# Kernel tuning notes

Measured on AMD Instinct MI355X. Metric: run time of the kernel, lower is better.

Reference implementation:

```python
import jax, jax.numpy as jnp
import numpy as np

K = 7        # upsample_kernel_size
S = 2        # upscale_factor
EK = K - 2   # encoder kernel size (5)


def conv2d(x, w, b, padding):
    out = jax.lax.conv_general_dilated(
        x, w, window_strides=(1, 1), padding=[(padding, padding), (padding, padding)],
        dimension_numbers=('NCHW', 'OIHW', 'NCHW'))
    return out + b[None, :, None, None]


def pixel_shuffle(x, s):
    B, C, H, W = x.shape
    oc = C // (s * s)
    x = x.reshape(B, oc, s, s, H, W)
    x = x.transpose(0, 1, 4, 2, 5, 3)
    return x.reshape(B, oc, H * s, W * s)


def carafe(x, kmap, k, s):
    # x: [B,C,H,W], kmap: [B,k*k,H*s,W*s] softmax-normalized
    B, C, H, W = x.shape
    pad = k // 2
    xp = jnp.pad(x, ((0, 0), (0, 0), (pad, pad), (pad, pad)))
    # k^2 shifted views -> [B,C,k2,H,W]
    patches = jnp.stack([xp[:, :, dy:dy + H, dx:dx + W]
                         for dy in range(k) for dx in range(k)], axis=2)
    # output pixel (i,j) reads source (i//s, j//s): factor kmap spatial dims
    km = kmap.reshape(B, k * k, H, s, W, s)
    out = jnp.einsum('bcnhw,bnhpwq->bchpwq', patches, km)
    return out.reshape(B, C, H * s, W * s)


def setup_inputs() -> dict:
    key = jax.random.key(0)
    k1, k2, k3 = jax.random.split(key, 3)
    B, C, H, W = 4, 256, 64, 64
    comp_c = 64
    enc_out = (S * K) ** 2  # 196
    x = jax.random.normal(k1, (B, C, H, W), dtype=jnp.float32)
    w_comp = jax.random.normal(k2, (comp_c, C, 1, 1), dtype=jnp.float32) * (1.0 / np.sqrt(C))
    b_comp = jnp.zeros((comp_c,), dtype=jnp.float32)
    w_enc = jax.random.normal(k3, (enc_out, comp_c, EK, EK), dtype=jnp.float32) * (1.0 / np.sqrt(comp_c * EK * EK))
    b_enc = jnp.zeros((enc_out,), dtype=jnp.float32)
    return {'x': x, 'w_comp': w_comp, 'b_comp': b_comp, 'w_enc': w_enc, 'b_enc': b_enc}


def reference(x, w_comp, b_comp, w_enc, b_enc):
    compressed = conv2d(x, w_comp, b_comp, padding=0)
    content = conv2d(compressed, w_enc, b_enc, padding=EK // 2)
    upsampled = pixel_shuffle(content, S)            # [B, k^2, H*s, W*s]
    kernel_map = jax.nn.softmax(upsampled, axis=1)
    return carafe(x, kernel_map, K, S)
```

## Files before the change

kernel.cpp:

```cpp
#include <hip/hip_runtime.h>
#include <math.h>
#include <stdint.h>

#define B_   4
#define C_   256
#define H_   64
#define W_   64
#define CC_  64
#define OE_  196
#define OH_  128
#define OW_  128
#define XH_  72
#define NWB_ 10

typedef uint32_t u32;
typedef unsigned short u16;
typedef __attribute__((ext_vector_type(8))) short bf16x8;
typedef __attribute__((ext_vector_type(4))) float f32x4;
typedef __attribute__((ext_vector_type(4))) u32 u32x4;
typedef __attribute__((ext_vector_type(2))) u32 u32x2;

__device__ __forceinline__ u16 f2bf(float f) {
  u32 u = __builtin_bit_cast(u32, f);
  u32 r = (u + 0x7FFFu + ((u >> 16) & 1u)) >> 16;
  return (u16)r;
}

__global__ __launch_bounds__(256) void prep_weights(
    const float* __restrict__ w_comp, const float* __restrict__ w_enc,
    u16* __restrict__ wfrag, u16* __restrict__ wcf,
    u16* __restrict__ xw8) {
  int idx = blockIdx.x * 256 + threadIdx.x;
  if (idx < 50 * 14 * 64) {
    int lane = idx & 63;
    int mt   = (idx >> 6) % 14;
    int ks   = idx / (14 * 64);
    int o    = mt * 16 + (lane & 15);
    int tap  = ks >> 1, s = ks & 1;
    int ky   = tap / 5, kx = tap % 5;
    int cb   = s * 32 + (lane >> 4) * 8;
    u32 pk[4];
    #pragma unroll
    for (int p = 0; p < 4; ++p) {
      u16 lo = 0, hi = 0;
      if (o < OE_) {
        lo = f2bf(w_enc[((o * CC_ + cb + 2 * p) * 5 + ky) * 5 + kx]);
        hi = f2bf(w_enc[((o * CC_ + cb + 2 * p + 1) * 5 + ky) * 5 + kx]);
      }
      pk[p] = (u32)lo | ((u32)hi << 16);
    }
    *reinterpret_cast<u32x4*>(wfrag + (size_t)idx * 8) =
        *reinterpret_cast<u32x4*>(pk);
  }
  if (idx < 8 * 4 * 64) {
    int lane = idx & 63;
    int mt   = (idx >> 6) & 3;
    int ks   = idx >> 8;
    int o    = mt * 16 + (lane & 15);
    int cb   = ks * 32 + (lane >> 4) * 8;
    u32 pk[4];
    #pragma unroll
    for (int p = 0; p < 4; ++p) {
      u16 lo = f2bf(w_comp[o * C_ + cb + 2 * p]);
      u16 hi = f2bf(w_comp[o * C_ + cb + 2 * p + 1]);
      pk[p] = (u32)lo | ((u32)hi << 16);
    }
    *reinterpret_cast<u32x4*>(wcf + (size_t)idx * 8) =
        *reinterpret_cast<u32x4*>(pk);
  }
  {
    u32x4 z = {0, 0, 0, 0};
    for (int i = idx; i < 1088 * 256; i += 65536) {
      int zi = i >> 8, ck = i & 255;
      int b = zi / 272, r = zi % 272;
      int hp, wb;
      if (r < 30)      { hp = r / 10;             wb = r % 10; }
      else if (r < 80) { hp = 67 + (r - 30) / 10; wb = (r - 30) % 10; }
      else {
        int rr = r - 80;
        hp = 3 + rr / 3;
        int m = rr % 3;
        wb = (m == 0) ? 0 : (m == 1) ? 8 : 9;
      }
      *reinterpret_cast<u32x4*>(
          xw8 + (((size_t)(b * XH_ + hp)) * NWB_ + wb) * (C_ * 8) + ck * 8) = z;
    }
  }
}

__global__ __launch_bounds__(256) void compress_k(
    const float* __restrict__ x, const u16* __restrict__ wcf,
    const float* __restrict__ b_comp, u16* __restrict__ comp,
    u16* __restrict__ xw8) {
  __shared__ float xs[C_ * 20];
  int t   = threadIdx.x;
  int gid = blockIdx.x;
  int wq  = gid & 3;
  int bh  = gid >> 2;
  int b = bh >> 6, h = bh & 63;
  int w0 = wq * 16;

  const float* xrow = x + (size_t)b * C_ * H_ * W_ + (size_t)h * W_ + w0;
  for (int i = t; i < 1024; i += 256) {
    int c = i >> 2, q = i & 3;
    f32x4 v = *reinterpret_cast<const f32x4*>(xrow + (size_t)c * H_ * W_ + q * 4);
    *reinterpret_cast<f32x4*>(xs + c * 20 + q * 4) = v;
  }
  __syncthreads();

  int wv   = __builtin_amdgcn_readfirstlane(t >> 6);
  int lane = t & 63;
  int w    = lane & 15;
  int lg   = lane >> 4;

  bf16x8 af[8];
  #pragma unroll
  for (int ks = 0; ks < 8; ++ks)
    af[ks] = *reinterpret_cast<const bf16x8*>(
        wcf + (((size_t)ks * 4 + wv) * 64 + lane) * 8);

  f32x4 acc = {0.f, 0.f, 0.f, 0.f};
  #pragma unroll
  for (int ks = 0; ks < 8; ++ks) {
    short vv[8];
    #pragma unroll
    for (int j = 0; j < 8; ++j)
      vv[j] = (short)f2bf(xs[(ks * 32 + lg * 8 + j) * 20 + w]);
    bf16x8 bf = (bf16x8){vv[0], vv[1], vv[2], vv[3], vv[4], vv[5], vv[6], vv[7]};
    acc = __builtin_amdgcn_mfma_f32_16x16x32_bf16(af[ks], bf, acc, 0, 0, 0);
  }

  {
    int cc0 = wv * 16 + lg * 4;
    f32x4 bias = *reinterpret_cast<const f32x4*>(b_comp + cc0);
    u32 p0 = (u32)f2bf(acc[0] + bias[0]) | ((u32)f2bf(acc[1] + bias[1]) << 16);
    u32 p1 = (u32)f2bf(acc[2] + bias[2]) | ((u32)f2bf(acc[3] + bias[3]) << 16);
    u32x2 pk = {p0, p1};
    *reinterpret_cast<u32x2*>(comp + ((size_t)bh * 64 + w0 + w) * CC_ + cc0) = pk;
  }

  {
    int ww = t & 15, cq = t >> 4;
    int wp = w0 + ww + 3;
    size_t base = (((size_t)(b * XH_ + h + 3)) * NWB_ + (wp >> 3)) * (C_ * 8) + (wp & 7);
    #pragma unroll
    for (int i = 0; i < 16; ++i) {
      int c = cq * 16 + i;
      xw8[base + c * 8] = f2bf(xs[c * 20 + ww]);
    }
  }
}

#define ELG_ 32256

__device__ __forceinline__ void enc_lda(
    bf16x8 (&a)[2], const u16* __restrict__ wfrag,
    int ks, int mtbase, int lane) {
  #pragma unroll
  for (int mm = 0; mm < 2; ++mm)
    a[mm] = *reinterpret_cast<const bf16x8*>(
        wfrag + (((size_t)ks * 14 + mtbase + mm) * 64 + lane) * 8);
}

__device__ __forceinline__ void enc_step(
    int ks, const char* lds, const bf16x8 (&a)[2], f32x4 (&acc)[2][2],
    int nlane, int kq) {
  int tap = ks >> 1, s = ks & 1;
  int ky = tap / 5, kx = tap % 5;
  bf16x8 bf[2];
  #pragma unroll
  for (int nt = 0; nt < 2; ++nt) {
    int col = nt * 16 + nlane + kx;
    int byte = (((ky * 36 + col) * 64 + s * 32 + kq * 8) * 2) ^ ((col & 7) << 4);
    bf[nt] = *reinterpret_cast<const bf16x8*>(lds + byte);
  }
  #pragma unroll
  for (int mm = 0; mm < 2; ++mm)
    #pragma unroll
    for (int nt = 0; nt < 2; ++nt)
      acc[mm][nt] = __builtin_amdgcn_mfma_f32_16x16x32_bf16(
          a[mm], bf[nt], acc[mm][nt], 0, 0, 0);
}

__global__ __launch_bounds__(512) void enc_mfma_k(
    const u16* __restrict__ comp, const u16* __restrict__ wfrag,
    const float* __restrict__ b_enc, u16* __restrict__ smax) {
  __shared__ __align__(16) char lds[ELG_];

  int t   = threadIdx.x;
  int bid = blockIdx.x;
  int swz = (bid & 7) * 64 + (bid >> 3);
  int wh  = swz & 1;
  int bh  = swz >> 1;
  int b = bh >> 6, h = bh & 63;
  int w0 = wh * 32;

  {
    const u16* cbse = comp + (size_t)b * H_ * W_ * CC_;
    for (int i = t; i < 1440; i += 512) {
      int q = i & 7, colr = i >> 3;
      int col = colr % 36, r = colr / 36;
      int hh = h - 2 + r, gw = w0 - 2 + col;
      u32x4 v = {0, 0, 0, 0};
      if ((unsigned)hh < H_ && (unsigned)gw < W_)
        v = *reinterpret_cast<const u32x4*>(cbse + ((size_t)hh * W_ + gw) * CC_ + q * 8);
      int byte = ((r * 36 + col) * 128 + q * 16) ^ ((col & 7) << 4);
      *reinterpret_cast<u32x4*>(lds + byte) = v;
    }
  }
  __syncthreads();

  int wv    = __builtin_amdgcn_readfirstlane(t >> 6);
  int lane  = t & 63;
  int nlane = lane & 15, kq = lane >> 4;
  int mtbase = wv * 2;

  f32x4 acc[2][2];
  #pragma unroll
  for (int mm = 0; mm < 2; ++mm)
    #pragma unroll
    for (int nt = 0; nt < 2; ++nt) acc[mm][nt] = (f32x4){0.f, 0.f, 0.f, 0.f};

  if (wv < 7) {
    bf16x8 abuf[4][2];
    #pragma unroll
    for (int p = 0; p < 4; ++p) enc_lda(abuf[p], wfrag, p, mtbase, lane);
    #pragma unroll
    for (int ks = 0; ks < 50; ++ks) {
      enc_step(ks, lds, abuf[ks & 3], acc, nlane, kq);
      if (ks < 46) enc_lda(abuf[ks & 3], wfrag, ks + 4, mtbase, lane);
    }
  }

  __syncthreads();
  float* lg = (float*)lds;
  if (wv < 7) {
    #pragma unroll
    for (int mm = 0; mm < 2; ++mm) {
      #pragma unroll
      for (int nt = 0; nt < 2; ++nt) {
        #pragma unroll
        for (int r = 0; r < 4; ++r) {
          int m  = (mtbase + mm) * 16 + kq * 4 + r;
          int px = nt * 16 + nlane;
          lg[m * 36 + px] = acc[mm][nt][r] + (m < OE_ ? b_enc[m] : 0.f);
        }
      }
    }
  }
  __syncthreads();

  if (t < 128) {
    int px = t & 31, rr = t >> 5;
    float v[49];
    float mx = -1e30f;
    #pragma unroll
    for (int n = 0; n < 49; ++n) {
      v[n] = lg[(4 * n + rr) * 36 + px];
      mx = fmaxf(mx, v[n]);
    }
    float sum = 0.f;
    #pragma unroll
    for (int n = 0; n < 49; ++n) { v[n] = __expf(v[n] - mx); sum += v[n]; }
    float inv = 1.f / sum;
    u16* so = smax + ((size_t)bh * 64 + w0 + px) * OE_;
    #pragma unroll
    for (int n = 0; n < 49; ++n) so[n * 4 + rr] = f2bf(v[n] * inv);
  }
}

__device__ __forceinline__ void carafe_lda(
    bf16x8 (&buf)[4], const u16* __restrict__ xb,
    int c, int h, int wb0, int lg) {
  #pragma unroll
  for (int ks = 0; ks < 4; ++ks) {
    int dy = ks * 2 + (lg >> 1);
    buf[ks] = *reinterpret_cast<const bf16x8*>(
        xb + (((size_t)(h + dy)) * NWB_ + wb0 + (lg & 1)) * (C_ * 8) + c * 8);
  }
}

__global__ __launch_bounds__(256) void carafe_k(
    const u16* __restrict__ xw8, const u16* __restrict__ smax,
    float* __restrict__ out) {
  __shared__ __align__(8) u16 svl[16 * 200];
  int t   = threadIdx.x;
  int bid = blockIdx.x;
  int swz = (bid & 7) * 256 + (bid >> 3);
  int mh  = swz & 1;
  int ws2 = (swz >> 1) & 3;
  int h   = (swz >> 3) & 63;
  int b   = swz >> 9;
  int w00 = ws2 * 16;

  for (int idx = t; idx < 784; idx += 256) {
    int pix = idx / 49, n = idx - pix * 49;
    const u16* sp = smax +
        ((size_t)((b * 64 + h) * 64) + w00 + pix) * OE_ + n * 4;
    *reinterpret_cast<u32x2*>(svl + pix * 200 + n * 4) =
        *reinterpret_cast<const u32x2*>(sp);
  }
  __syncthreads();

  int wv   = t >> 6;
  int lane = t & 63;
  int ws   = wv & 1;
  int mq   = wv >> 1;
  int w0   = w00 + ws * 8;
  int wb0  = w0 >> 3;
  const u16* svb = svl + ws * 8 * 200;

  int col = lane & 15;
  int wi  = col >> 1, q = col & 1;
  int lg  = lane >> 4;
  int mrow = lane & 15;

  bf16x8 bfr[2][4];
  #pragma unroll
  for (int p = 0; p < 2; ++p) {
    #pragma unroll
    for (int ks = 0; ks < 4; ++ks) {
      short v[8];
      #pragma unroll
      for (int j = 0; j < 8; ++j) {
        int k   = ks * 32 + lg * 8 + j;
        int dy  = k >> 4, dxp = k & 15;
        int dx  = dxp - wi;
        u16 s = 0;
        if (dy < 7 && dx >= 0 && dx < 7)
          s = svb[wi * 200 + (dy * 7 + dx) * 4 + 2 * p + q];
        v[j] = (short)s;
      }
      bfr[p][ks] = (bf16x8){v[0], v[1], v[2], v[3], v[4], v[5], v[6], v[7]};
    }
  }

  const u16* xb = xw8 + (size_t)b * XH_ * NWB_ * (C_ * 8);
  int mt0 = mh * 8 + mq * 4;
  bf16x8 buf[4][4];
  #pragma unroll
  for (int i = 0; i < 4; ++i)
    carafe_lda(buf[i], xb, (mt0 + i) * 16 + mrow, h, wb0, lg);

  #pragma unroll
  for (int i = 0; i < 4; ++i) {
    int mt = mt0 + i;
    f32x4 acc0 = {0.f, 0.f, 0.f, 0.f};
    f32x4 acc1 = {0.f, 0.f, 0.f, 0.f};
    #pragma unroll
    for (int ks = 0; ks < 4; ++ks) {
      acc0 = __builtin_amdgcn_mfma_f32_16x16x32_bf16(buf[i][ks], bfr[0][ks], acc0, 0, 0, 0);
      acc1 = __builtin_amdgcn_mfma_f32_16x16x32_bf16(buf[i][ks], bfr[1][ks], acc1, 0, 0, 0);
    }
    float* o0 = out +
        ((size_t)(b * C_ + mt * 16 + lg * 4) * OH_ + 2 * h) * OW_ + 2 * w0 + col;
    o0[0]                     = acc0[0];
    o0[(size_t)OH_ * OW_]     = acc0[1];
    o0[2 * (size_t)OH_ * OW_] = acc0[2];
    o0[3 * (size_t)OH_ * OW_] = acc0[3];
    float* o1 = o0 + OW_;
    o1[0]                     = acc1[0];
    o1[(size_t)OH_ * OW_]     = acc1[1];
    o1[2 * (size_t)OH_ * OW_] = acc1[2];
    o1[3 * (size_t)OH_ * OW_] = acc1[3];
  }
}

extern "C" void kernel_launch(void* const* d_in, const int* in_sizes, int n_in,
                              void* d_out, int out_size, void* d_ws, size_t ws_size,
                              hipStream_t stream) {
  const float* x      = (const float*)d_in[0];
  const float* w_comp = (const float*)d_in[1];
  const float* b_comp = (const float*)d_in[2];
  const float* w_enc  = (const float*)d_in[3];
  const float* b_enc  = (const float*)d_in[4];
  float* out = (float*)d_out;

  u16* smax  = (u16*)d_ws;
  u16* wfrag = smax + 3211264;
  u16* wcf   = wfrag + 358400;
  u16* comp  = wcf + 16384;
  u16* xw8   = comp + 1048576;

  prep_weights<<<256, 256, 0, stream>>>(w_comp, w_enc, wfrag, wcf, xw8);
  compress_k<<<B_ * H_ * 4, 256, 0, stream>>>(x, wcf, b_comp, comp, xw8);
  enc_mfma_k<<<512, 512, 0, stream>>>(comp, wfrag, b_enc, smax);
  carafe_k<<<2048, 256, 0, stream>>>(xw8, smax, out);
}
```

Before: 68.65 us.

## Emit MFMA-ready B fragments from encoder softmax and double-buffer carafe A loads

The encoder kernel now writes softmax weights directly in the per-lane bf16x8 fragment layout that carafe's MFMA B operand needs, expanding the 7x7 window into a zero-padded 16-wide band. This removes carafe's LDS staging, its barrier and the per-element gather logic. The cost is a larger workspace write (about 2.6x more data than the compact softmax) and an extra barrier in the encoder. Carafe also switches from preloading all four A tiles to a two-buffer prefetch, which lowers register pressure.

Result: faster. 65.68 us (-4.3%).

```diff
diff --git a/kernel.cpp b/kernel.cpp
--- a/kernel.cpp
+++ b/kernel.cpp
@@ -184,7 +184,7 @@
 
 __global__ __launch_bounds__(512) void enc_mfma_k(
     const u16* __restrict__ comp, const u16* __restrict__ wfrag,
-    const float* __restrict__ b_enc, u16* __restrict__ smax) {
+    const float* __restrict__ b_enc, u16* __restrict__ bfrB) {
   __shared__ __align__(16) char lds[ELG_];
 
   int t   = threadIdx.x;
@@ -250,9 +250,10 @@
   }
   __syncthreads();
 
+  float v[49];
+  float inv = 0.f;
   if (t < 128) {
     int px = t & 31, rr = t >> 5;
-    float v[49];
     float mx = -1e30f;
     #pragma unroll
     for (int n = 0; n < 49; ++n) {
@@ -262,95 +263,108 @@
     float sum = 0.f;
     #pragma unroll
     for (int n = 0; n < 49; ++n) { v[n] = __expf(v[n] - mx); sum += v[n]; }
-    float inv = 1.f / sum;
-    u16* so = smax + ((size_t)bh * 64 + w0 + px) * OE_;
-    #pragma unroll
-    for (int n = 0; n < 49; ++n) so[n * 4 + rr] = f2bf(v[n] * inv);
+    inv = 1.f / sum;
+  }
+  __syncthreads();
+
+  if (t < 128) {
+    int px = t & 31, rr = t >> 5;
+    u16* sva = (u16*)lds;
+    int myo = (px * 4 + rr) * 49;
+    #pragma unroll
+    for (int n = 0; n < 49; ++n) sva[myo + n] = f2bf(v[n] * inv);
+
+    int wi = px & 7, wg = wh * 4 + (px >> 3);
+    int p = rr >> 1, q = rr & 1;
+    size_t bb = ((((size_t)(b * 64 + h) * 8 + wg) * 2 + p) * 4) * 512 +
+                (size_t)(wi * 2 + q) * 8;
+    #pragma unroll
+    for (int ks = 0; ks < 4; ++ks) {
+      #pragma unroll
+      for (int lg2 = 0; lg2 < 4; ++lg2) {
+        u32 pk[4];
+        #pragma unroll
+        for (int jp = 0; jp < 4; ++jp) {
+          u16 e[2];
+          #pragma unroll
+          for (int u = 0; u < 2; ++u) {
+            int j  = jp * 2 + u;
+            int k  = ks * 32 + lg2 * 8 + j;
+            int dy = k >> 4, dxp = k & 15;
+            int dx = dxp - wi;
+            bool ok = (dy < 7) && (dx >= 0) && (dx < 7);
+            int idx = ok ? (dy * 7 + dx) : 0;
+            u16 s = sva[myo + idx];
+            e[u] = ok ? s : (u16)0;
+          }
+          pk[jp] = (u32)e[0] | ((u32)e[1] << 16);
+        }
+        *reinterpret_cast<u32x4*>(bfrB + bb + (size_t)ks * 512 + lg2 * 128) =
+            *reinterpret_cast<u32x4*>(pk);
+      }
+    }
   }
 }
 
 __device__ __forceinline__ void carafe_lda(
     bf16x8 (&buf)[4], const u16* __restrict__ xb,
-    int c, int h, int wb0, int lg) {
+    int c, int h, int wg, int lg) {
   #pragma unroll
   for (int ks = 0; ks < 4; ++ks) {
     int dy = ks * 2 + (lg >> 1);
     buf[ks] = *reinterpret_cast<const bf16x8*>(
-        xb + (((size_t)(h + dy)) * NWB_ + wb0 + (lg & 1)) * (C_ * 8) + c * 8);
+        xb + (((size_t)(h + dy)) * NWB_ + wg + (lg & 1)) * (C_ * 8) + c * 8);
   }
 }
 
 __global__ __launch_bounds__(256) void carafe_k(
-    const u16* __restrict__ xw8, const u16* __restrict__ smax,
+    const u16* __restrict__ xw8, const u16* __restrict__ bfrB,
     float* __restrict__ out) {
-  __shared__ __align__(8) u16 svl[16 * 200];
   int t   = threadIdx.x;
   int bid = blockIdx.x;
   int swz = (bid & 7) * 256 + (bid >> 3);
   int mh  = swz & 1;
-  int ws2 = (swz >> 1) & 3;
+  int wgp = (swz >> 1) & 3;
   int h   = (swz >> 3) & 63;
   int b   = swz >> 9;
-  int w00 = ws2 * 16;
-
-  for (int idx = t; idx < 784; idx += 256) {
-    int pix = idx / 49, n = idx - pix * 49;
-    const u16* sp = smax +
-        ((size_t)((b * 64 + h) * 64) + w00 + pix) * OE_ + n * 4;
-    *reinterpret_cast<u32x2*>(svl + pix * 200 + n * 4) =
-        *reinterpret_cast<const u32x2*>(sp);
-  }
-  __syncthreads();
 
   int wv   = t >> 6;
   int lane = t & 63;
-  int ws   = wv & 1;
+  int wg   = wgp * 2 + (wv & 1);
   int mq   = wv >> 1;
-  int w0   = w00 + ws * 8;
-  int wb0  = w0 >> 3;
-  const u16* svb = svl + ws * 8 * 200;
-
-  int col = lane & 15;
-  int wi  = col >> 1, q = col & 1;
-  int lg  = lane >> 4;
+  int mt0  = mh * 8 + mq * 4;
+  int col  = lane & 15;
+  int lg   = lane >> 4;
   int mrow = lane & 15;
-
-  bf16x8 bfr[2][4];
-  #pragma unroll
-  for (int p = 0; p < 2; ++p) {
-    #pragma unroll
-    for (int ks = 0; ks < 4; ++ks) {
-      short v[8];
-      #pragma unroll
-      for (int j = 0; j < 8; ++j) {
-        int k   = ks * 32 + lg * 8 + j;
-        int dy  = k >> 4, dxp = k & 15;
-        int dx  = dxp - wi;
-        u16 s = 0;
-        if (dy < 7 && dx >= 0 && dx < 7)
-          s = svb[wi * 200 + (dy * 7 + dx) * 4 + 2 * p + q];
-        v[j] = (short)s;
-      }
-      bfr[p][ks] = (bf16x8){v[0], v[1], v[2], v[3], v[4], v[5], v[6], v[7]};
-    }
-  }
+  int w0   = wg * 8;
+
+  bf16x8 bfp[2][4];
+  size_t bbase = (((size_t)(b * 64 + h) * 8 + wg) * 2) * 4 * 512;
+  #pragma unroll
+  for (int p = 0; p < 2; ++p)
+    #pragma unroll
+    for (int ks = 0; ks < 4; ++ks)
+      bfp[p][ks] = *reinterpret_cast<const bf16x8*>(
+          bfrB + bbase + (size_t)(p * 4 + ks) * 512 + lane * 8);
 
   const u16* xb = xw8 + (size_t)b * XH_ * NWB_ * (C_ * 8);
-  int mt0 = mh * 8 + mq * 4;
-  bf16x8 buf[4][4];
-  #pragma unroll
-  for (int i = 0; i < 4; ++i)
-    carafe_lda(buf[i], xb, (mt0 + i) * 16 + mrow, h, wb0, lg);
+  bf16x8 bufA[4], bufB[4];
+  carafe_lda(bufA, xb, mt0 * 16 + mrow, h, wg, lg);
 
   #pragma unroll
   for (int i = 0; i < 4; ++i) {
     int mt = mt0 + i;
+    if (i < 3) {
+      if (i & 1) carafe_lda(bufA, xb, (mt + 1) * 16 + mrow, h, wg, lg);
+      else       carafe_lda(bufB, xb, (mt + 1) * 16 + mrow, h, wg, lg);
+    }
     f32x4 acc0 = {0.f, 0.f, 0.f, 0.f};
     f32x4 acc1 = {0.f, 0.f, 0.f, 0.f};
     #pragma unroll
     for (int ks = 0; ks < 4; ++ks) {
-      acc0 = __builtin_amdgcn_mfma_f32_16x16x32_bf16(buf[i][ks], bfr[0][ks], acc0, 0, 0, 0);
-      acc1 = __builtin_amdgcn_mfma_f32_16x16x32_bf16(buf[i][ks], bfr[1][ks], acc1, 0, 0, 0);
+      bf16x8 af = (i & 1) ? bufB[ks] : bufA[ks];
+      acc0 = __builtin_amdgcn_mfma_f32_16x16x32_bf16(af, bfp[0][ks], acc0, 0, 0, 0);
+      acc1 = __builtin_amdgcn_mfma_f32_16x16x32_bf16(af, bfp[1][ks], acc1, 0, 0, 0);
     }
     float* o0 = out +
         ((size_t)(b * C_ + mt * 16 + lg * 4) * OH_ + 2 * h) * OW_ + 2 * w0 + col;
@@ -376,14 +390,14 @@
   const float* b_enc  = (const float*)d_in[4];
   float* out = (float*)d_out;
 
-  u16* smax  = (u16*)d_ws;
-  u16* wfrag = smax + 3211264;
+  u16* bfrB  = (u16*)d_ws;
+  u16* wfrag = bfrB + 8388608;
   u16* wcf   = wfrag + 358400;
   u16* comp  = wcf + 16384;
   u16* xw8   = comp + 1048576;
 
   prep_weights<<<256, 256, 0, stream>>>(w_comp, w_enc, wfrag, wcf, xw8);
   compress_k<<<B_ * H_ * 4, 256, 0, stream>>>(x, wcf, b_comp, comp, xw8);
-  enc_mfma_k<<<512, 512, 0, stream>>>(comp, wfrag, b_enc, smax);
-  carafe_k<<<2048, 256, 0, stream>>>(xw8, smax, out);
-}
+  enc_mfma_k<<<512, 512, 0, stream>>>(comp, wfrag, b_enc, bfrB);
+  carafe_k<<<2048, 256, 0, stream>>>(xw8, bfrB, out);
+}
```
